# Optimization experiments

Hardware: AMD Instinct MI355X
Metric: run time of the kernel (lower is better)

The kernel has to match this reference:

```python
import jax, jax.numpy as jnp
import numpy as np

HIDDEN = 1024
NUM_HEAD = 16
HEAD_DIM = HIDDEN // NUM_HEAD
VOCAB = 32000
MAX_LEN = 1024
EMBED = 512
BATCH = 4
SEQ = MAX_LEN  # mask broadcasting requires seq == max_len


def setup_inputs() -> dict:
    key = jax.random.key(0)
    ks = jax.random.split(key, 12)
    std = 0.02
    inp = {
        'input_ids': jax.random.randint(ks[0], (BATCH, SEQ), 0, VOCAB),
        'W_word': jax.random.normal(ks[1], (VOCAB, EMBED), jnp.float32) * std,
        'W_pos': jax.random.normal(ks[2], (MAX_LEN, EMBED), jnp.float32) * std,
        'Wq': jax.random.normal(ks[3], (HIDDEN, HIDDEN), jnp.float32) * std,
        'Wk': jax.random.normal(ks[4], (HIDDEN, HIDDEN), jnp.float32) * std,
        'Wv': jax.random.normal(ks[5], (HIDDEN, HIDDEN), jnp.float32) * std,
        'Wo': jax.random.normal(ks[6], (HIDDEN, HIDDEN), jnp.float32) * std,
        'W1': jax.random.normal(ks[7], (4 * HIDDEN, HIDDEN), jnp.float32) * std,
        'W2': jax.random.normal(ks[8], (HIDDEN, 4 * HIDDEN), jnp.float32) * std,
        'W_eh': jax.random.normal(ks[9], (HIDDEN, EMBED), jnp.float32) * std,
        'W_he': jax.random.normal(ks[10], (EMBED, HIDDEN), jnp.float32) * std,
        'W_lm': jax.random.normal(ks[11], (VOCAB, EMBED), jnp.float32) * std,
    }
    return inp


def reference(input_ids, W_word, W_pos, Wq, Wk, Wv, Wo, W1, W2, W_eh, W_he, W_lm):
    B, S = input_ids.shape
    # embeddings
    h = W_word[input_ids] + W_pos[jnp.arange(S)][None, :, :]  # [B,S,E]
    h = h @ W_eh.T  # embed -> hidden, [B,S,H]
    residual = h
    # QKV projections (Linear with weight [out,in]: y = x @ W.T)
    q = (h @ Wq.T).reshape(B, S, NUM_HEAD, HEAD_DIM).transpose(0, 2, 1, 3)
    k = (h @ Wk.T).reshape(B, S, NUM_HEAD, HEAD_DIM).transpose(0, 2, 1, 3)
    v = (h @ Wv.T).reshape(B, S, NUM_HEAD, HEAD_DIM).transpose(0, 2, 1, 3)
    # note: original scales by sqrt(hidden_size), NOT sqrt(head_dim)
    scores = jnp.einsum('bhqd,bhkd->bhqk', q, k) / jnp.sqrt(jnp.float32(HIDDEN))
    mask = jnp.tril(jnp.ones((S, S), dtype=bool))[None, None]
    scores = jnp.where(mask, scores, jnp.finfo(jnp.float32).min)
    attn = jax.nn.softmax(scores.astype(jnp.float32), axis=-1)
    out = jnp.einsum('bhqk,bhkd->bhqd', attn, v)
    out = out.transpose(0, 2, 1, 3).reshape(B, S, HIDDEN)
    h = residual + out @ Wo.T
    # MLP
    residual = h
    x = jax.nn.relu(h @ W1.T)
    h = residual + x @ W2.T
    # hidden -> embed, lm head
    h = h @ W_he.T
    logits = h @ W_lm.T  # [B,S,VOCAB]
    return logits
```

## Files before the change

### kernel.cpp

```cpp
#include <hip/hip_runtime.h>
#include <hip/hip_bf16.h>

#define HIDDEN 1024
#define NHEAD 16
#define HDIM 64
#define VOCAB 32000
#define SEQLEN 1024
#define EMBED 512
#define BATCH 4
#define ROWS (BATCH*SEQLEN)

typedef __bf16 bf16x8 __attribute__((ext_vector_type(8)));
typedef float f32x4 __attribute__((ext_vector_type(4)));
typedef unsigned short u16;

#define MFMA(a_, b_, c_) __builtin_amdgcn_mfma_f32_16x16x32_bf16(a_, b_, c_, 0, 0, 0)

#define VMCNT4 asm volatile("s_waitcnt vmcnt(4)" ::: "memory")
#define VMCNT0 asm volatile("s_waitcnt vmcnt(0)" ::: "memory")
#define LGKM0  asm volatile("s_waitcnt lgkmcnt(0)" ::: "memory")
#define CFENCE asm volatile("" ::: "memory")
#define SBAR   __builtin_amdgcn_s_barrier()
#define SCHEDB __builtin_amdgcn_sched_barrier(0)

__device__ __forceinline__ u16 f2bf(float f) {
  unsigned u = __builtin_bit_cast(unsigned, f);
  u = u + 0x7FFFu + ((u >> 16) & 1u);
  return (u16)(u >> 16);
}
__device__ __forceinline__ float bf2f(u16 s) {
  unsigned u = (unsigned)s << 16;
  return __builtin_bit_cast(float, u);
}

#define GLDS(g_, l_) __builtin_amdgcn_global_load_lds( \
    (const __attribute__((address_space(1))) void*)(g_), \
    (__attribute__((address_space(3))) void*)(l_), 16, 0, 0)

struct Prep {
  const float* src[8]; u16* dst[8];
  const float* wlm; u16* wlm_dst;
  const int* ids; const float* wword; const float* wpos; u16* h0b;
};
__global__ void prep_kernel(Prep pp) {
  int b = blockIdx.x;
  if (b < 13312) {
    int seg, off;
    if (b < 4096)        { seg = b >> 10; off = b & 1023; }
    else if (b < 8192)   { seg = 4; off = b - 4096; }
    else if (b < 12288)  { seg = 5; off = b - 8192; }
    else if (b < 12800)  { seg = 6; off = b - 12288; }
    else                 { seg = 7; off = b - 12800; }
    size_t i = ((size_t)off * 256 + threadIdx.x) * 4;
    float4 v = *(const float4*)(pp.src[seg] + i);
    unsigned a = f2bf(v.x) | ((unsigned)f2bf(v.y) << 16);
    unsigned d = f2bf(v.z) | ((unsigned)f2bf(v.w) << 16);
    *(uint2*)(pp.dst[seg] + i) = make_uint2(a, d);
  } else if (b < 29312) {
    if (!pp.wlm_dst) return;
    int off = b - 13312;
    size_t i = ((size_t)off * 256 + threadIdx.x) * 4;
    float4 v = *(const float4*)(pp.wlm + i);
    unsigned a = f2bf(v.x) | ((unsigned)f2bf(v.y) << 16);
    unsigned d = f2bf(v.z) | ((unsigned)f2bf(v.w) << 16);
    *(uint2*)(pp.wlm_dst + i) = make_uint2(a, d);
  } else {
    int off = b - 29312;
    int row = off * 2 + (threadIdx.x >> 7);
    int e = (threadIdx.x & 127) * 4;
    int s = row & (SEQLEN - 1);
    int id = pp.ids[row];
    float4 a = *(const float4*)(pp.wword + (size_t)id * EMBED + e);
    float4 c = *(const float4*)(pp.wpos + (size_t)s * EMBED + e);
    unsigned lo = f2bf(a.x + c.x) | ((unsigned)f2bf(a.y + c.y) << 16);
    unsigned hi = f2bf(a.z + c.z) | ((unsigned)f2bf(a.w + c.w) << 16);
    *(uint2*)(pp.h0b + (size_t)row * EMBED + e) = make_uint2(lo, hi);
  }
}

template<int EPI, bool WF32, bool WB16, bool BF32, bool SWZ, bool NT, int BN>
__global__ __launch_bounds__(256, 2) void gemm128(
    const u16* __restrict__ A, const u16* __restrict__ Bb,
    const float* __restrict__ Bf,
    float* __restrict__ C, u16* __restrict__ Cb,
    const u16* __restrict__ R, int K, int ldc)
{
  constexpr int NF  = BN / 32;
  constexpr int BCH = BN / 32;
  __shared__ __align__(16) u16 smem[16384 + 2 * BN * 64];
  u16* As0 = &smem[0];
  u16* As1 = &smem[8192];
  u16* Bs0 = &smem[16384];
  u16* Bs1 = &smem[16384 + BN * 64];

  int tid = threadIdx.x;
  int lane = tid & 63, wave = tid >> 6;
  int wr = wave >> 1, wc = wave & 1;
  int cl = lane & 15, gp = (lane >> 4) & 3;

  int bx = blockIdx.x, by = blockIdx.y;
  if (SWZ) {
    int nwg = gridDim.x * gridDim.y;
    int flat = by * gridDim.x + bx;
    int cpx = nwg >> 3;
    int swz = (flat & 7) * cpx + (flat >> 3);
    bx = swz % gridDim.x; by = swz / gridDim.x;
  }
  int m0 = bx * 128, n0 = by * BN;

  int srow8 = lane >> 3;
  int scol = (((lane & 7) - srow8) & 7) * 8;
  int pos0 = ((gp + cl) & 7) * 8;
  int pos1 = ((gp + cl + 4) & 7) * 8;

  f32x4 acc[4][NF] = {};
  int nk = K >> 6;

  #pragma unroll
  for (int i = 0; i < 4; ++i) {
    int c = i * 4 + wave;
    GLDS(A + (size_t)(m0 + c * 8 + srow8) * K + scol, As0 + c * 512);
  }
  if (!BF32) {
    #pragma unroll
    for (int i = 0; i < BCH; ++i) {
      int c = i * 4 + wave;
      GLDS(Bb + (size_t)(n0 + c * 8 + srow8) * K + scol, Bs0 + c * 512);
    }
  } else {
    #pragma unroll
    for (int it = 0; it < BN / 32; ++it) {
      int idx = it * 256 + tid;
      int row = idx >> 3, p = idx & 7;
      int gc = (p - row) & 7;
      const float* src = Bf + (size_t)(n0 + row) * K + gc * 8;
      float4 v0 = *(const float4*)src, v1 = *(const float4*)(src + 4);
      union { bf16x8 v; u16 s[8]; } u;
      u.s[0]=f2bf(v0.x); u.s[1]=f2bf(v0.y); u.s[2]=f2bf(v0.z); u.s[3]=f2bf(v0.w);
      u.s[4]=f2bf(v1.x); u.s[5]=f2bf(v1.y); u.s[6]=f2bf(v1.z); u.s[7]=f2bf(v1.w);
      *(bf16x8*)&Bs0[row * 64 + p * 8] = u.v;
    }
  }

  for (int kt = 0; kt < nk; ++kt) {
    int buf = kt & 1;
    u16* Asb = buf ? As1 : As0;
    u16* Bsb = buf ? Bs1 : Bs0;
    u16* Asn = buf ? As0 : As1;
    u16* Bsn = buf ? Bs0 : Bs1;
    int kb = (kt + 1) << 6;
    bool more = kt + 1 < nk;

    if (more) {
      #pragma unroll
      for (int i = 0; i < 4; ++i) {
        int c = i * 4 + wave;
        GLDS(A + (size_t)(m0 + c * 8 + srow8) * K + kb + scol, Asn + c * 512);
      }
    }
    if (BF32) { VMCNT0; } else if (more) { VMCNT4; } else { VMCNT0; }
    SCHEDB;
    SBAR;
    CFENCE; SCHEDB;

    bf16x8 af[4][2], bfv[NF][2];
    #pragma unroll
    for (int n = 0; n < NF; ++n) {
      int r = (wc * (BN / 2) + n * 16 + cl) * 64;
      bfv[n][0] = *(const bf16x8*)&Bsb[r + pos0];
      bfv[n][1] = *(const bf16x8*)&Bsb[r + pos1];
    }
    #pragma unroll
    for (int m = 0; m < 4; ++m) {
      int r = (wr * 64 + m * 16 + cl) * 64;
      af[m][0] = *(const bf16x8*)&Asb[r + pos0];
      af[m][1] = *(const bf16x8*)&Asb[r + pos1];
    }

    __builtin_amdgcn_s_setprio(1);
    #pragma unroll
    for (int m = 0; m < 2; ++m)
      #pragma unroll
      for (int n = 0; n < NF; ++n)
        #pragma unroll
        for (int ks = 0; ks < 2; ++ks)
          acc[m][n] = MFMA(af[m][ks], bfv[n][ks], acc[m][n]);
    __builtin_amdgcn_s_setprio(0);

    if (more) {
      if (!BF32) {
        #pragma unroll
        for (int i = 0; i < BCH; ++i) {
          int c = i * 4 + wave;
          GLDS(Bb + (size_t)(n0 + c * 8 + srow8) * K + kb + scol, Bsn + c * 512);
        }
      } else {
        #pragma unroll
        for (int it = 0; it < BN / 32; ++it) {
          int idx = it * 256 + tid;
          int row = idx >> 3, p = idx & 7;
          int gc = (p - row) & 7;
          const float* src = Bf + (size_t)(n0 + row) * K + kb + gc * 8;
          float4 v0 = *(const float4*)src, v1 = *(const float4*)(src + 4);
          union { bf16x8 v; u16 s[8]; } u;
          u.s[0]=f2bf(v0.x); u.s[1]=f2bf(v0.y); u.s[2]=f2bf(v0.z); u.s[3]=f2bf(v0.w);
          u.s[4]=f2bf(v1.x); u.s[5]=f2bf(v1.y); u.s[6]=f2bf(v1.z); u.s[7]=f2bf(v1.w);
          *(bf16x8*)&Bsn[row * 64 + p * 8] = u.v;
        }
      }
    }

    __builtin_amdgcn_s_setprio(1);
    #pragma unroll
    for (int n = 0; n < NF; ++n)
      #pragma unroll
      for (int ks = 0; ks < 2; ++ks)
        acc[2][n] = MFMA(af[2][ks], bfv[n][ks], acc[2][n]);
    __builtin_amdgcn_s_setprio(0);

    LGKM0;
    SCHEDB;
    SBAR;
    CFENCE; SCHEDB;

    __builtin_amdgcn_s_setprio(1);
    #pragma unroll
    for (int n = 0; n < NF; ++n)
      #pragma unroll
      for (int ks = 0; ks < 2; ++ks)
        acc[3][n] = MFMA(af[3][ks], bfv[n][ks], acc[3][n]);
    __builtin_amdgcn_s_setprio(0);
  }

  if constexpr (WF32 && !WB16 && BN == 128) {
    float* Cst = (float*)&smem[0];
    __syncthreads();
    #pragma unroll
    for (int g = 0; g < 2; ++g) {
      if (wr == g) {
        #pragma unroll
        for (int m = 0; m < 4; ++m)
          #pragma unroll
          for (int n = 0; n < 4; ++n)
            #pragma unroll
            for (int j = 0; j < 4; ++j)
              Cst[(m * 16 + gp * 4 + j) * 132 + wc * 64 + n * 16 + cl] = acc[m][n][j];
      }
      __syncthreads();
      int r2 = lane >> 5, cw = lane & 31;
      #pragma unroll
      for (int p = 0; p < 8; ++p) {
        int r = p * 8 + wave * 2 + r2;
        int grow = m0 + g * 64 + r;
        f32x4 v = *(f32x4*)&Cst[r * 132 + cw * 4];
        if constexpr (EPI == 1) {
          ushort4 rv = *(const ushort4*)&R[(size_t)grow * ldc + n0 + cw * 4];
          v[0] += bf2f(rv.x); v[1] += bf2f(rv.y); v[2] += bf2f(rv.z); v[3] += bf2f(rv.w);
        }
        if constexpr (EPI == 2) {
          #pragma unroll
          for (int j = 0; j < 4; ++j) v[j] = fmaxf(v[j], 0.f);
        }
        if (NT) __builtin_nontemporal_store(v, (f32x4*)&C[(size_t)grow * ldc + n0 + cw * 4]);
        else *(f32x4*)&C[(size_t)grow * ldc + n0 + cw * 4] = v;
      }
      __syncthreads();
    }
  } else {
    int r0 = gp * 4;
    #pragma unroll
    for (int m = 0; m < 4; ++m) {
      #pragma unroll
      for (int n = 0; n < NF; ++n) {
        int col = n0 + wc * (BN / 2) + n * 16 + cl;
        #pragma unroll
        for (int j = 0; j < 4; ++j) {
          int row = m0 + wr * 64 + m * 16 + r0 + j;
          float v = acc[m][n][j];
          if (EPI == 1) v += bf2f(R[(size_t)row * ldc + col]);
          if (EPI == 2) v = fmaxf(v, 0.f);
          if (WF32) C[(size_t)row * ldc + col] = v;
          if (WB16) Cb[(size_t)row * ldc + col] = f2bf(v);
        }
      }
    }
  }
}

template<int EPI, bool WF32, bool WB16, bool SWZ, bool NT = false>
__global__ __launch_bounds__(512) void gemm256(
    const u16* __restrict__ A, const u16* __restrict__ B,
    float* __restrict__ C, u16* __restrict__ Cb,
    const u16* __restrict__ R, int K, int ldc)
{
  __shared__ __align__(16) u16 smem[4][256 * 64];
  int tid = threadIdx.x;
  int lane = tid & 63, wave = tid >> 6;
  int wr = wave >> 2, wc = wave & 3;
  int cl = lane & 15, gp = (lane >> 4) & 3;

  int bx = blockIdx.x, by = blockIdx.y;
  if (SWZ) {
    int nwg = gridDim.x * gridDim.y;
    int flat = by * gridDim.x + bx;
    int cpx = nwg >> 3;
    int swz = (flat & 7) * cpx + (flat >> 3);
    bx = swz % gridDim.x; by = swz / gridDim.x;
  }
  int m0 = bx * 256, n0 = by * 256;

  int srow8 = lane >> 3;
  int scol = (((lane & 7) - srow8) & 7) * 8;
  int pos0 = ((gp + cl) & 7) * 8;
  int pos1 = ((gp + cl + 4) & 7) * 8;

  f32x4 acc[8][4] = {};
  int nk = K >> 6;

  #pragma unroll
  for (int i = 0; i < 4; ++i) {
    int c = i * 8 + wave;
    GLDS(A + (size_t)(m0 + c * 8 + srow8) * K + scol, &smem[0][c * 512]);
  }
  #pragma unroll
  for (int i = 0; i < 4; ++i) {
    int c = i * 8 + wave;
    GLDS(B + (size_t)(n0 + c * 8 + srow8) * K + scol, &smem[2][c * 512]);
  }

  for (int kt = 0; kt < nk; ++kt) {
    int buf = kt & 1;
    int kb = (kt + 1) << 6;
    bool more = kt + 1 < nk;

    if (more) {
      #pragma unroll
      for (int i = 0; i < 4; ++i) {
        int c = i * 8 + wave;
        GLDS(A + (size_t)(m0 + c * 8 + srow8) * K + kb + scol, &smem[buf ^ 1][c * 512]);
      }
      VMCNT4;
    } else {
      VMCNT0;
    }
    SCHEDB;
    SBAR;
    CFENCE; SCHEDB;

    bf16x8 af0[4][2], af1[4][2], bf0[2][2], bf1[2][2];
    #pragma unroll
    for (int n = 0; n < 2; ++n) {
      int r = (wc * 64 + n * 16 + cl) * 64;
      bf0[n][0] = *(const bf16x8*)&smem[2 + buf][r + pos0];
      bf0[n][1] = *(const bf16x8*)&smem[2 + buf][r + pos1];
    }
    #pragma unroll
    for (int m = 0; m < 4; ++m) {
      int r = (wr * 128 + m * 16 + cl) * 64;
      af0[m][0] = *(const bf16x8*)&smem[buf][r + pos0];
      af0[m][1] = *(const bf16x8*)&smem[buf][r + pos1];
    }
    #pragma unroll
    for (int n = 0; n < 2; ++n) {
      int r = (wc * 64 + (n + 2) * 16 + cl) * 64;
      bf1[n][0] = *(const bf16x8*)&smem[2 + buf][r + pos0];
      bf1[n][1] = *(const bf16x8*)&smem[2 + buf][r + pos1];
    }
    #pragma unroll
    for (int m = 0; m < 4; ++m) {
      int r = (wr * 128 + (m + 4) * 16 + cl) * 64;
      af1[m][0] = *(const bf16x8*)&smem[buf][r + pos0];
      af1[m][1] = *(const bf16x8*)&smem[buf][r + pos1];
    }

    __builtin_amdgcn_s_setprio(1);
    #pragma unroll
    for (int m = 0; m < 4; ++m)
      #pragma unroll
      for (int n = 0; n < 2; ++n)
        #pragma unroll
        for (int ks = 0; ks < 2; ++ks)
          acc[m][n] = MFMA(af0[m][ks], bf0[n][ks], acc[m][n]);
    __builtin_amdgcn_s_setprio(0);

    if (more) {
      #pragma unroll
      for (int i = 0; i < 4; ++i) {
        int c = i * 8 + wave;
        GLDS(B + (size_t)(n0 + c * 8 + srow8) * K + kb + scol, &smem[2 + (buf ^ 1)][c * 512]);
      }
    }

    __builtin_amdgcn_s_setprio(1);
    #pragma unroll
    for (int m = 0; m < 4; ++m)
      #pragma unroll
      for (int n = 0; n < 2; ++n)
        #pragma unroll
        for (int ks = 0; ks < 2; ++ks)
          acc[m][n + 2] = MFMA(af0[m][ks], bf1[n][ks], acc[m][n + 2]);
    __builtin_amdgcn_s_setprio(0);

    LGKM0;
    SCHEDB;
    SBAR;
    CFENCE; SCHEDB;

    __builtin_amdgcn_s_setprio(1);
    #pragma unroll
    for (int m = 0; m < 4; ++m)
      #pragma unroll
      for (int n = 0; n < 2; ++n)
        #pragma unroll
        for (int ks = 0; ks < 2; ++ks)
          acc[m + 4][n] = MFMA(af1[m][ks], bf0[n][ks], acc[m + 4][n]);
    #pragma unroll
    for (int m = 0; m < 4; ++m)
      #pragma unroll
      for (int n = 0; n < 2; ++n)
        #pragma unroll
        for (int ks = 0; ks < 2; ++ks)
          acc[m + 4][n + 2] = MFMA(af1[m][ks], bf1[n][ks], acc[m + 4][n + 2]);
    __builtin_amdgcn_s_setprio(0);
  }

  if constexpr (WF32 && !WB16) {
    float* Cst = (float*)&smem[0][0];
    __syncthreads();
    #pragma unroll
    for (int g = 0; g < 4; ++g) {
      if ((g >> 1) == wr) {
        #pragma unroll
        for (int k = 0; k < 4; ++k) {
          int ar = (g & 1) * 4 + k;
          int rl = ar * 16 + gp * 4 - (g & 1) * 64;
          #pragma unroll
          for (int n = 0; n < 4; ++n) {
            int col = wc * 64 + n * 16 + cl;
            #pragma unroll
            for (int j = 0; j < 4; ++j)
              Cst[(rl + j) * 260 + col] = acc[ar][n][j];
          }
        }
      }
      __syncthreads();
      #pragma unroll
      for (int p = 0; p < 8; ++p) {
        int r = p * 8 + wave;
        int c4 = lane * 4;
        int grow = m0 + g * 64 + r;
        f32x4 v = *(f32x4*)&Cst[r * 260 + c4];
        if constexpr (EPI == 1) {
          ushort4 rv = *(const ushort4*)&R[(size_t)grow * ldc + n0 + c4];
          v[0] += bf2f(rv.x); v[1] += bf2f(rv.y); v[2] += bf2f(rv.z); v[3] += bf2f(rv.w);
        }
        if constexpr (EPI == 2) {
          #pragma unroll
          for (int j = 0; j < 4; ++j) v[j] = fmaxf(v[j], 0.f);
        }
        if (NT) __builtin_nontemporal_store(v, (f32x4*)&C[(size_t)grow * ldc + n0 + c4]);
        else *(f32x4*)&C[(size_t)grow * ldc + n0 + c4] = v;
      }
      __syncthreads();
    }
  } else {
    int r0 = gp * 4;
    #pragma unroll
    for (int m = 0; m < 8; ++m) {
      #pragma unroll
      for (int n = 0; n < 4; ++n) {
        int col = n0 + wc * 64 + n * 16 + cl;
        #pragma unroll
        for (int j = 0; j < 4; ++j) {
          int row = m0 + wr * 128 + m * 16 + r0 + j;
          float v = acc[m][n][j];
          if (EPI == 1) v += bf2f(R[(size_t)row * ldc + col]);
          if (EPI == 2) v = fmaxf(v, 0.f);
          if (WF32) C[(size_t)row * ldc + col] = v;
          if (WB16) Cb[(size_t)row * ldc + col] = f2bf(v);
        }
      }
    }
  }
}

#define LSTR 72
__global__ __launch_bounds__(256) void attn_kernel(const u16* __restrict__ qkv,
                                                   u16* __restrict__ outb) {
  __shared__ u16 Ksm[2][64 * 64];
  __shared__ u16 Vsm[2][64 * LSTR];
  __shared__ u16 Psm[64 * LSTR];
  int pi = blockIdx.x, h = blockIdx.y, b = blockIdx.z;
  int qbA = pi, qbB = 15 - pi;
  int tid = threadIdx.x;
  int lane = tid & 63, wave = tid >> 6;
  int cl = lane & 15, gp = lane >> 4;
  int srow8 = lane >> 3;
  int gsrc = (((lane & 7) - srow8) & 7) * 8;

  const u16* base = qkv + (size_t)b * SEQLEN * (3 * HIDDEN);

  bf16x8 qA0, qA1, qB0, qB1;
  {
    const u16* qp = base + (size_t)(qbA * 64 + wave * 16 + cl) * (3 * HIDDEN) + h * HDIM;
    qA0 = *(const bf16x8*)(qp + gp * 8);
    qA1 = *(const bf16x8*)(qp + 32 + gp * 8);
    const u16* qq = base + (size_t)(qbB * 64 + wave * 16 + cl) * (3 * HIDDEN) + h * HDIM;
    qB0 = *(const bf16x8*)(qq + gp * 8);
    qB1 = *(const bf16x8*)(qq + 32 + gp * 8);
  }

  ushort4 vr[4];
  auto stageK = [&](int t, int bb) {
    #pragma unroll
    for (int i = 0; i < 2; ++i) {
      int c = wave * 2 + i;
      int row = c * 8 + srow8;
      GLDS(base + (size_t)(t * 64 + row) * (3 * HIDDEN) + HIDDEN + h * HDIM + gsrc,
           &Ksm[bb][c * 512]);
    }
  };
  auto loadV = [&](int t) {
    #pragma unroll
    for (int it = 0; it < 4; ++it) {
      int idx = it * 256 + tid;
      int row = idx >> 4, c4 = (idx & 15) * 4;
      vr[it] = *(const ushort4*)(base + (size_t)(t * 64 + row) * (3 * HIDDEN) +
                                 2 * HIDDEN + h * HDIM + c4);
    }
  };
  auto writeV = [&](int bb) {
    #pragma unroll
    for (int it = 0; it < 4; ++it) {
      int idx = it * 256 + tid;
      int row = idx >> 4, c4 = (idx & 15) * 4;
      Vsm[bb][(c4 + 0) * LSTR + row] = vr[it].x;
      Vsm[bb][(c4 + 1) * LSTR + row] = vr[it].y;
      Vsm[bb][(c4 + 2) * LSTR + row] = vr[it].z;
      Vsm[bb][(c4 + 3) * LSTR + row] = vr[it].w;
    }
  };

  float mA[4], lA[4], mB[4], lB[4];
  f32x4 oA[4] = {}, oB[4] = {};
  #pragma unroll
  for (int j = 0; j < 4; ++j) { mA[j] = -INFINITY; lA[j] = 0.f; mB[j] = -INFINITY; lB[j] = 0.f; }

  auto stateStep = [&](int t, int buf, int qb, bf16x8 q0, bf16x8 q1,
                       float* mrow, float* lrow, f32x4* oacc) {
    f32x4 sfr[4];
    __builtin_amdgcn_s_setprio(1);
    #pragma unroll
    for (int n = 0; n < 4; ++n) {
      f32x4 z = {};
      bf16x8 kf0 = *(const bf16x8*)&Ksm[buf][(n * 16 + cl) * 64 + ((gp + cl) & 7) * 8];
      bf16x8 kf1 = *(const bf16x8*)&Ksm[buf][(n * 16 + cl) * 64 + ((gp + cl + 4) & 7) * 8];
      z = MFMA(q0, kf0, z);
      z = MFMA(q1, kf1, z);
      sfr[n] = z;
    }
    __builtin_amdgcn_s_setprio(0);

    bool diag = (t == qb);
    #pragma unroll
    for (int n = 0; n < 4; ++n)
      #pragma unroll
      for (int j = 0; j < 4; ++j) {
        float sv = sfr[n][j] * 0.03125f;
        if (diag) {
          int lr = wave * 16 + gp * 4 + j;
          int lc = n * 16 + cl;
          sv = (lc <= lr) ? sv : -1e30f;
        }
        sfr[n][j] = sv;
      }
    float so[4];
    #pragma unroll
    for (int j = 0; j < 4; ++j) {
      float tm = fmaxf(fmaxf(sfr[0][j], sfr[1][j]), fmaxf(sfr[2][j], sfr[3][j]));
      tm = fmaxf(tm, __shfl_xor(tm, 1));
      tm = fmaxf(tm, __shfl_xor(tm, 2));
      tm = fmaxf(tm, __shfl_xor(tm, 4));
      tm = fmaxf(tm, __shfl_xor(tm, 8));
      float mn = fmaxf(mrow[j], tm);
      so[j] = __expf(mrow[j] - mn);
      mrow[j] = mn;
      float ts = 0.f;
      #pragma unroll
      for (int n = 0; n < 4; ++n) {
        float p = __expf(sfr[n][j] - mn);
        sfr[n][j] = p;
        ts += p;
      }
      ts += __shfl_xor(ts, 1); ts += __shfl_xor(ts, 2);
      ts += __shfl_xor(ts, 4); ts += __shfl_xor(ts, 8);
      lrow[j] = lrow[j] * so[j] + ts;
    }
    #pragma unroll
    for (int n = 0; n < 4; ++n)
      #pragma unroll
      for (int j = 0; j < 4; ++j)
        oacc[n][j] *= so[j];

    #pragma unroll
    for (int n = 0; n < 4; ++n)
      #pragma unroll
      for (int j = 0; j < 4; ++j)
        Psm[(wave * 16 + gp * 4 + j) * LSTR + n * 16 + cl] = f2bf(sfr[n][j]);
    __builtin_amdgcn_sched_barrier(0);

    bf16x8 pa0 = *(const bf16x8*)&Psm[(wave * 16 + cl) * LSTR + gp * 8];
    bf16x8 pa1 = *(const bf16x8*)&Psm[(wave * 16 + cl) * LSTR + 32 + gp * 8];
    __builtin_amdgcn_s_setprio(1);
    #pragma unroll
    for (int n = 0; n < 4; ++n) {
      bf16x8 vb0 = *(const bf16x8*)&Vsm[buf][(n * 16 + cl) * LSTR + gp * 8];
      bf16x8 vb1 = *(const bf16x8*)&Vsm[buf][(n * 16 + cl) * LSTR + 32 + gp * 8];
      oacc[n] = MFMA(pa0, vb0, oacc[n]);
      oacc[n] = MFMA(pa1, vb1, oacc[n]);
    }
    __builtin_amdgcn_s_setprio(0);
  };

  stageK(0, 0);
  loadV(0);
  writeV(0);
  __syncthreads();

  for (int t = 0; t <= qbB; ++t) {
    int buf = t & 1;
    bool more = t < qbB;
    if (more) { stageK(t + 1, buf ^ 1); loadV(t + 1); }

    stateStep(t, buf, qbB, qB0, qB1, mB, lB, oB);
    if (more) writeV(buf ^ 1);
    if (t <= qbA)
      stateStep(t, buf, qbA, qA0, qA1, mA, lA, oA);

    __syncthreads();
  }

  #pragma unroll
  for (int n = 0; n < 4; ++n)
    #pragma unroll
    for (int j = 0; j < 4; ++j) {
      int lr = wave * 16 + gp * 4 + j;
      int d = n * 16 + cl;
      outb[(size_t)(b * SEQLEN + qbA * 64 + lr) * HIDDEN + h * HDIM + d] = f2bf(oA[n][j] / lA[j]);
      outb[(size_t)(b * SEQLEN + qbB * 64 + lr) * HIDDEN + h * HDIM + d] = f2bf(oB[n][j] / lB[j]);
    }
}

extern "C" void kernel_launch(void* const* d_in, const int* in_sizes, int n_in,
                              void* d_out, int out_size, void* d_ws, size_t ws_size,
                              hipStream_t stream) {
  const int*   ids    = (const int*)d_in[0];
  const float* W_word = (const float*)d_in[1];
  const float* W_pos  = (const float*)d_in[2];
  const float* Wq     = (const float*)d_in[3];
  const float* Wk     = (const float*)d_in[4];
  const float* Wv     = (const float*)d_in[5];
  const float* Wo     = (const float*)d_in[6];
  const float* W1     = (const float*)d_in[7];
  const float* W2     = (const float*)d_in[8];
  const float* W_eh   = (const float*)d_in[9];
  const float* W_he   = (const float*)d_in[10];
  const float* W_lm   = (const float*)d_in[11];
  float* out = (float*)d_out;
  char*  ob  = (char*)d_out;
  char*  wb  = (char*)d_ws;

  const size_t MB = 1024 * 1024;
  u16*   h0b   = (u16*)(ob + 32 * MB);
  u16*   h1b   = (u16*)(ob + 36 * MB);
  u16*   qkvb  = (u16*)(ob + 44 * MB);
  u16*   attnb = (u16*)(ob + 68 * MB);
  u16*   h2b   = (u16*)(ob + 76 * MB);
  u16*   xb    = (u16*)(ob + 84 * MB);
  u16*   h3b   = (u16*)(ob + 116 * MB);
  u16*   Wqkv_b= (u16*)(ob + 124 * MB);
  u16*   Wo_b  = (u16*)(ob + 130 * MB);
  u16*   W1_b  = (u16*)(ob + 132 * MB);
  u16*   W2_b  = (u16*)(ob + 140 * MB);
  u16*   Weh_b = (u16*)(ob + 148 * MB);
  u16*   Whe_b = (u16*)(ob + 149 * MB);
  u16*   he_b  = (u16*)(wb + 0);
  u16*   Wlm_b = (u16*)(wb + 4 * MB);
  bool big_ws = ws_size >= 36 * MB;

  Prep pp;
  pp.src[0] = Wq;  pp.dst[0] = Wqkv_b + 0 * 1024 * 1024;
  pp.src[1] = Wk;  pp.dst[1] = Wqkv_b + 1 * 1024 * 1024;
  pp.src[2] = Wv;  pp.dst[2] = Wqkv_b + 2 * 1024 * 1024;
  pp.src[3] = Wo;  pp.dst[3] = Wo_b;
  pp.src[4] = W1;  pp.dst[4] = W1_b;
  pp.src[5] = W2;  pp.dst[5] = W2_b;
  pp.src[6] = W_eh; pp.dst[6] = Weh_b;
  pp.src[7] = W_he; pp.dst[7] = Whe_b;
  pp.wlm = W_lm; pp.wlm_dst = big_ws ? Wlm_b : nullptr;
  pp.ids = ids; pp.wword = W_word; pp.wpos = W_pos; pp.h0b = h0b;
  prep_kernel<<<dim3(31360), 256, 0, stream>>>(pp);

  gemm128<0, false, true, false, false, false, 64><<<dim3(32, 16), 256, 0, stream>>>(
      h0b, Weh_b, nullptr, nullptr, h1b, nullptr, 512, HIDDEN);
  gemm128<0, false, true, false, false, false, 128><<<dim3(32, 24), 256, 0, stream>>>(
      h1b, Wqkv_b, nullptr, nullptr, qkvb, nullptr, 1024, 3 * HIDDEN);
  attn_kernel<<<dim3(8, 16, 4), 256, 0, stream>>>(qkvb, attnb);
  gemm128<1, false, true, false, false, false, 64><<<dim3(32, 16), 256, 0, stream>>>(
      attnb, Wo_b, nullptr, nullptr, h2b, h1b, 1024, HIDDEN);
  gemm256<2, false, true, false><<<dim3(16, 16), 512, 0, stream>>>(
      h2b, W1_b, nullptr, xb, nullptr, 1024, 4 * HIDDEN);
  gemm128<1, false, true, false, false, false, 64><<<dim3(32, 16), 256, 0, stream>>>(
      xb, W2_b, nullptr, nullptr, h3b, h2b, 4096, HIDDEN);
  gemm128<0, false, true, false, false, false, 64><<<dim3(32, 8), 256, 0, stream>>>(
      h3b, Whe_b, nullptr, nullptr, he_b, nullptr, 1024, EMBED);
  if (big_ws)
    gemm256<0, true, false, true, true><<<dim3(16, 125), 512, 0, stream>>>(
        he_b, Wlm_b, out, nullptr, nullptr, 512, VOCAB);
  else
    gemm128<0, true, false, true, true, true, 128><<<dim3(32, 250), 256, 0, stream>>>(
        he_b, nullptr, W_lm, out, nullptr, nullptr, 512, VOCAB);
}
```

Measured before the change: 404.6 us.

## Stage bf16 GEMM epilogues through LDS for coalesced stores, nontemporal weight prep

Adds LDS-staged epilogue paths for bf16-output GEMMs (QKV projection and W1+ReLU), so each wave writes full contiguous row segments instead of scattered 2-byte stores. Also turns on the swizzle template flag for the QKV and W2 GEMMs. The weight-conversion stores in the prep kernel become nontemporal. This reduces uncoalesced global writes, at the cost of extra LDS traffic and barriers in the epilogue.

```diff
diff --git a/kernel.cpp b/kernel.cpp
--- a/kernel.cpp
+++ b/kernel.cpp
@@ -12,6 +12,7 @@
 
 typedef __bf16 bf16x8 __attribute__((ext_vector_type(8)));
 typedef float f32x4 __attribute__((ext_vector_type(4)));
+typedef unsigned uu2 __attribute__((ext_vector_type(2)));
 typedef unsigned short u16;
 
 #define MFMA(a_, b_, c_) __builtin_amdgcn_mfma_f32_16x16x32_bf16(a_, b_, c_, 0, 0, 0)
@@ -53,17 +54,19 @@
     else                 { seg = 7; off = b - 12800; }
     size_t i = ((size_t)off * 256 + threadIdx.x) * 4;
     float4 v = *(const float4*)(pp.src[seg] + i);
-    unsigned a = f2bf(v.x) | ((unsigned)f2bf(v.y) << 16);
-    unsigned d = f2bf(v.z) | ((unsigned)f2bf(v.w) << 16);
-    *(uint2*)(pp.dst[seg] + i) = make_uint2(a, d);
+    uu2 w;
+    w[0] = f2bf(v.x) | ((unsigned)f2bf(v.y) << 16);
+    w[1] = f2bf(v.z) | ((unsigned)f2bf(v.w) << 16);
+    __builtin_nontemporal_store(w, (uu2*)(pp.dst[seg] + i));
   } else if (b < 29312) {
     if (!pp.wlm_dst) return;
     int off = b - 13312;
     size_t i = ((size_t)off * 256 + threadIdx.x) * 4;
     float4 v = *(const float4*)(pp.wlm + i);
-    unsigned a = f2bf(v.x) | ((unsigned)f2bf(v.y) << 16);
-    unsigned d = f2bf(v.z) | ((unsigned)f2bf(v.w) << 16);
-    *(uint2*)(pp.wlm_dst + i) = make_uint2(a, d);
+    uu2 w;
+    w[0] = f2bf(v.x) | ((unsigned)f2bf(v.y) << 16);
+    w[1] = f2bf(v.z) | ((unsigned)f2bf(v.w) << 16);
+    __builtin_nontemporal_store(w, (uu2*)(pp.wlm_dst + i));
   } else {
     int off = b - 29312;
     int row = off * 2 + (threadIdx.x >> 7);
@@ -266,6 +269,31 @@
       }
       __syncthreads();
     }
+  } else if constexpr (WB16 && !WF32 && BN == 128 && EPI == 0) {
+    u16* Cst = &smem[0];
+    __syncthreads();
+    #pragma unroll
+    for (int g = 0; g < 2; ++g) {
+      if (wr == g) {
+        #pragma unroll
+        for (int m = 0; m < 4; ++m)
+          #pragma unroll
+          for (int n = 0; n < 4; ++n)
+            #pragma unroll
+            for (int j = 0; j < 4; ++j)
+              Cst[(m * 16 + gp * 4 + j) * 132 + wc * 64 + n * 16 + cl] = f2bf(acc[m][n][j]);
+      }
+      __syncthreads();
+      int r2 = lane >> 5, cw = lane & 31;
+      #pragma unroll
+      for (int p = 0; p < 8; ++p) {
+        int r = p * 8 + wave * 2 + r2;
+        int grow = m0 + g * 64 + r;
+        ushort4 w = *(ushort4*)&Cst[r * 132 + cw * 4];
+        *(ushort4*)&Cb[(size_t)grow * ldc + n0 + cw * 4] = w;
+      }
+      __syncthreads();
+    }
   } else {
     int r0 = gp * 4;
     #pragma unroll
@@ -460,6 +488,38 @@
         }
         if (NT) __builtin_nontemporal_store(v, (f32x4*)&C[(size_t)grow * ldc + n0 + c4]);
         else *(f32x4*)&C[(size_t)grow * ldc + n0 + c4] = v;
+      }
+      __syncthreads();
+    }
+  } else if constexpr (WB16 && !WF32 && EPI != 1) {
+    u16* Cst = &smem[0][0];
+    __syncthreads();
+    #pragma unroll
+    for (int g = 0; g < 4; ++g) {
+      if ((g >> 1) == wr) {
+        #pragma unroll
+        for (int k = 0; k < 4; ++k) {
+          int ar = (g & 1) * 4 + k;
+          int rl = ar * 16 + gp * 4 - (g & 1) * 64;
+          #pragma unroll
+          for (int n = 0; n < 4; ++n) {
+            int col = wc * 64 + n * 16 + cl;
+            #pragma unroll
+            for (int j = 0; j < 4; ++j) {
+              float v = acc[ar][n][j];
+              if (EPI == 2) v = fmaxf(v, 0.f);
+              Cst[(rl + j) * 264 + col] = f2bf(v);
+            }
+          }
+        }
+      }
+      __syncthreads();
+      #pragma unroll
+      for (int p = 0; p < 8; ++p) {
+        int r = p * 8 + wave;
+        int grow = m0 + g * 64 + r;
+        ushort4 w = *(ushort4*)&Cst[r * 264 + lane * 4];
+        *(ushort4*)&Cb[(size_t)grow * ldc + n0 + lane * 4] = w;
       }
       __syncthreads();
     }
@@ -703,14 +763,14 @@
 
   gemm128<0, false, true, false, false, false, 64><<<dim3(32, 16), 256, 0, stream>>>(
       h0b, Weh_b, nullptr, nullptr, h1b, nullptr, 512, HIDDEN);
-  gemm128<0, false, true, false, false, false, 128><<<dim3(32, 24), 256, 0, stream>>>(
+  gemm128<0, false, true, false, true, false, 128><<<dim3(32, 24), 256, 0, stream>>>(
       h1b, Wqkv_b, nullptr, nullptr, qkvb, nullptr, 1024, 3 * HIDDEN);
   attn_kernel<<<dim3(8, 16, 4), 256, 0, stream>>>(qkvb, attnb);
   gemm128<1, false, true, false, false, false, 64><<<dim3(32, 16), 256, 0, stream>>>(
       attnb, Wo_b, nullptr, nullptr, h2b, h1b, 1024, HIDDEN);
-  gemm256<2, false, true, false><<<dim3(16, 16), 512, 0, stream>>>(
+  gemm256<2, false, true, true><<<dim3(16, 16), 512, 0, stream>>>(
       h2b, W1_b, nullptr, xb, nullptr, 1024, 4 * HIDDEN);
-  gemm128<1, false, true, false, false, false, 64><<<dim3(32, 16), 256, 0, stream>>>(
+  gemm128<1, false, true, false, true, false, 64><<<dim3(32, 16), 256, 0, stream>>>(
       xb, W2_b, nullptr, nullptr, h3b, h2b, 4096, HIDDEN);
   gemm128<0, false, true, false, false, false, 64><<<dim3(32, 8), 256, 0, stream>>>(
       h3b, Whe_b, nullptr, nullptr, he_b, nullptr, 1024, EMBED);
```

Measured after the change: 466.5 us. +15.3%, slower.
